# Optimization experiments

Measured on AMD Instinct MI355X. Metric: run time of the kernel, lower is better.

The kernel has to match this reference:

```python
import jax, jax.numpy as jnp
import numpy as np
from jax import lax

IMG_H = IMG_W = 800.0
PRE_NMS = 2000      # rpn_pre_nms_top_n (test)
POST_NMS = 1000     # rpn_post_nms_top_n (test)
IOU_THR = 0.7       # rpn nms_thresh
MIN_SIZE = 1e-3     # filter_proposals min_size
SCORE_THR = 0.0     # rpn score_thresh
BBOX_CLIP = float(np.log(1000.0 / 16.0))  # torchvision BoxCoder bbox_xform_clip


def setup_inputs() -> dict:
    key = jax.random.key(0)
    k1, k2, k3, k4 = jax.random.split(key, 4)
    N, A = 8, 1_000_000
    objectness = jax.random.normal(k1, (N, A), jnp.float32)
    deltas = jax.random.normal(k2, (N, A, 4), jnp.float32) * 0.5
    # realistic anchors: random centers inside the image, sizes in [16, 256]
    cxy = jax.random.uniform(k3, (A, 2), jnp.float32) * jnp.array([IMG_W, IMG_H], jnp.float32)
    wh = 16.0 + jax.random.uniform(k4, (A, 2), jnp.float32) * 240.0
    anchors = jnp.concatenate([cxy - 0.5 * wh, cxy + 0.5 * wh], axis=-1)
    return {"objectness": objectness, "deltas": deltas, "anchors": anchors}


def decode_boxes(deltas, anchors):
    # torchvision BoxCoder.decode_single with weights (1,1,1,1)
    wa = anchors[:, 2] - anchors[:, 0]          # [A]
    ha = anchors[:, 3] - anchors[:, 1]
    cxa = anchors[:, 0] + 0.5 * wa
    cya = anchors[:, 1] + 0.5 * ha
    dx, dy = deltas[..., 0], deltas[..., 1]      # [N, A]
    dw = jnp.minimum(deltas[..., 2], BBOX_CLIP)
    dh = jnp.minimum(deltas[..., 3], BBOX_CLIP)
    pcx = dx * wa + cxa
    pcy = dy * ha + cya
    pw = jnp.exp(dw) * wa
    ph = jnp.exp(dh) * ha
    return jnp.stack([pcx - 0.5 * pw, pcy - 0.5 * ph,
                      pcx + 0.5 * pw, pcy + 0.5 * ph], axis=-1)  # [N, A, 4]


def nms_keep(boxes, valid):
    # greedy NMS on score-sorted boxes [K,4]; returns boolean keep mask [K]
    K = boxes.shape[0]
    areas = (boxes[:, 2] - boxes[:, 0]) * (boxes[:, 3] - boxes[:, 1])
    idxs = jnp.arange(K)

    def body(i, keep):
        xx1 = jnp.maximum(boxes[i, 0], boxes[:, 0])
        yy1 = jnp.maximum(boxes[i, 1], boxes[:, 1])
        xx2 = jnp.minimum(boxes[i, 2], boxes[:, 2])
        yy2 = jnp.minimum(boxes[i, 3], boxes[:, 3])
        inter = jnp.maximum(xx2 - xx1, 0.0) * jnp.maximum(yy2 - yy1, 0.0)
        iou = inter / (areas[i] + areas - inter + 1e-12)
        sup = (iou > IOU_THR) & (idxs > i) & keep[i]
        return keep & ~sup

    return lax.fori_loop(0, K, body, valid)


def filter_one(obj, boxes):
    # per-image filter_proposals: top-k -> sigmoid -> clip -> small-box removal -> NMS -> top post_nms
    top_logits, idx = lax.top_k(obj, PRE_NMS)        # sorted desc; sigmoid is monotone
    b = boxes[idx]                                    # [K, 4]
    scores = jax.nn.sigmoid(top_logits)
    x1 = jnp.clip(b[:, 0], 0.0, IMG_W)
    y1 = jnp.clip(b[:, 1], 0.0, IMG_H)
    x2 = jnp.clip(b[:, 2], 0.0, IMG_W)
    y2 = jnp.clip(b[:, 3], 0.0, IMG_H)
    bc = jnp.stack([x1, y1, x2, y2], axis=-1)
    valid = ((x2 - x1) >= MIN_SIZE) & ((y2 - y1) >= MIN_SIZE) & (scores > SCORE_THR)
    keep = nms_keep(lax.stop_gradient(bc), valid)     # selection is non-differentiable
    masked = jnp.where(keep, scores, -jnp.inf)
    _, fidx = lax.top_k(lax.stop_gradient(masked), POST_NMS)
    out_boxes = bc[fidx]                              # [POST_NMS, 4]
    out_scores = jnp.where(keep[fidx], scores[fidx], 0.0)
    return out_boxes, out_scores


def reference(objectness, deltas, anchors):
    proposals = decode_boxes(deltas, anchors)                 # [N, A, 4]
    boxes, scores = jax.vmap(filter_one)(objectness, proposals)
    return jnp.concatenate([boxes, scores[:, :, None]], axis=-1)  # [N, POST_NMS, 5]
```

## Files before the change

kernel.cpp:

```cpp
#include <hip/hip_runtime.h>
#include <cstdint>

#define NIMG 8
#define PRE 2000
#define POST 1000
#define NCH 128
#define CH_CAP 128
#define CAND_TOT (NCH*CH_CAP)
#define NSORT 4
#define GPS (NCH/NSORT)
#define SEG 2048
#define CAND_MAX (NSORT*SEG)
#define NPB 64
#define PB_CAP 1024
#define PAIR_CAP 12288
#define JT 256
#define IMGW 800.0f
#define BBOX_CLIP_F 4.135166556742356f
#define STATIC_KMIN 0xC0200000u

#define OFF_BCNT  0
#define OFF_DONE  (OFF_BCNT + NIMG*NCH*4)
#define OFF_BPCNT (OFF_DONE + 1024)
#define OFF_CAND  (OFF_BPCNT + NIMG*NPB*4)
#define OFF_SRT   (OFF_CAND + (size_t)NIMG*CAND_TOT*8)
#define OFF_BOX   (OFF_SRT + (size_t)NIMG*CAND_MAX*8)
#define OFF_SCORE (OFF_BOX + (size_t)NIMG*PRE*16)
#define OFF_VALID (OFF_SCORE + NIMG*PRE*4)
#define OFF_PAIRS (OFF_VALID + NIMG*PRE*4)

__device__ __forceinline__ unsigned int fkey(float f) {
    unsigned int b = __float_as_uint(f);
    return (b & 0x80000000u) ? ~b : (b | 0x80000000u);
}
__device__ __forceinline__ float inv_fkey(unsigned int k) {
    unsigned int b = (k & 0x80000000u) ? (k ^ 0x80000000u) : ~k;
    return __uint_as_float(b);
}

__global__ void k_compact(const float* __restrict__ obj,
                          unsigned long long* __restrict__ cand,
                          unsigned int* __restrict__ bcnt,
                          unsigned int* __restrict__ done, int A) {
    __shared__ unsigned long long loc[CH_CAP];
    __shared__ unsigned int lcnt;
    const int img = blockIdx.y;
    const int b = blockIdx.x;
    const int t = threadIdx.x;
    if (t == 0) {
        lcnt = 0u;
        if (b == 0) done[img * 32] = 0u;
    }
    __syncthreads();
    const float4* p4 = (const float4*)(obj + (size_t)img * A);
    const int nvec = A >> 2;
    for (int i = b * 256 + t; i < nvec; i += NCH * 256) {
        float4 v = p4[i];
        unsigned int k0 = fkey(v.x), k1 = fkey(v.y), k2 = fkey(v.z), k3 = fkey(v.w);
        unsigned int base = (unsigned int)(i << 2);
        if (k0 >= STATIC_KMIN) { unsigned int p = atomicAdd(&lcnt, 1u); if (p < CH_CAP) loc[p] = ((unsigned long long)k0 << 32) | (0xFFFFFFFFu - base); }
        if (k1 >= STATIC_KMIN) { unsigned int p = atomicAdd(&lcnt, 1u); if (p < CH_CAP) loc[p] = ((unsigned long long)k1 << 32) | (0xFFFFFFFFu - (base + 1u)); }
        if (k2 >= STATIC_KMIN) { unsigned int p = atomicAdd(&lcnt, 1u); if (p < CH_CAP) loc[p] = ((unsigned long long)k2 << 32) | (0xFFFFFFFFu - (base + 2u)); }
        if (k3 >= STATIC_KMIN) { unsigned int p = atomicAdd(&lcnt, 1u); if (p < CH_CAP) loc[p] = ((unsigned long long)k3 << 32) | (0xFFFFFFFFu - (base + 3u)); }
    }
    if (b == 0) {
        const float* p = obj + (size_t)img * A;
        for (int i = (nvec << 2) + t; i < A; i += 256) {
            unsigned int k = fkey(p[i]);
            if (k >= STATIC_KMIN) { unsigned int q = atomicAdd(&lcnt, 1u); if (q < CH_CAP) loc[q] = ((unsigned long long)k << 32) | (0xFFFFFFFFu - (unsigned int)i); }
        }
    }
    __syncthreads();
    if (t == 0) bcnt[img * NCH + b] = lcnt;
    unsigned int n = min(lcnt, (unsigned int)CH_CAP);
    unsigned long long* dst = cand + (size_t)img * CAND_TOT + (size_t)b * CH_CAP;
    for (unsigned int i = t; i < n; i += 256) dst[i] = loc[i];
}

__global__ __launch_bounds__(1024) void k_sortmerge(
    const float* __restrict__ obj, const float* __restrict__ deltas, const float* __restrict__ anchors,
    unsigned long long* __restrict__ cand, const unsigned int* __restrict__ bcnt,
    unsigned long long* __restrict__ srt, unsigned int* __restrict__ done,
    float* __restrict__ boxes, float* __restrict__ scores, unsigned int* __restrict__ valid, int A) {
    __shared__ unsigned long long sb[3 * SEG];
    __shared__ unsigned int cnts[NCH];
    __shared__ unsigned int pref[GPS + 1];
    __shared__ unsigned int kth_s, lcnt;
    __shared__ int bad_s;
    const int img = blockIdx.y;
    const int myseg = blockIdx.x;
    const int t = threadIdx.x;

    if (t < NCH) cnts[t] = bcnt[img * NCH + t];
    __syncthreads();
    if (t == 0) {
        int bad = 0; unsigned int tot = 0;
        for (int c = 0; c < NCH; ++c) { unsigned int r = cnts[c]; if (r > CH_CAP) bad = 1; tot += min(r, (unsigned int)CH_CAP); }
        for (int g = 0; g < NSORT; ++g) {
            unsigned int s = 0;
            for (int c = 0; c < GPS; ++c) s += min(cnts[g * GPS + c], (unsigned int)CH_CAP);
            if (s > (unsigned int)SEG) bad = 1;
        }
        if (tot < (unsigned int)PRE) bad = 1;
        bad_s = bad;
        if (!bad) {
            unsigned int o = 0; pref[0] = 0;
            for (int c = 0; c < GPS; ++c) { o += min(cnts[myseg * GPS + c], (unsigned int)CH_CAP); pref[c + 1] = o; }
        }
    }
    __syncthreads();

    for (int i = t; i < SEG; i += 1024) sb[i] = 0ull;
    __syncthreads();

    if (!bad_s) {
        const int c = t >> 5, lane = t & 31;
        const unsigned int b0 = pref[c], n = pref[c + 1] - pref[c];
        const unsigned long long* src = cand + (size_t)img * CAND_TOT + (size_t)(myseg * GPS + c) * CH_CAP;
        for (unsigned int i = lane; i < n; i += 32) sb[b0 + i] = src[i];
    } else {
        unsigned int* h = (unsigned int*)sb;
        for (int i = t; i < 4096; i += 1024) h[i] = 0u;
        __syncthreads();
        const float* p = obj + (size_t)img * A;
        for (int i = t; i < A; i += 1024) atomicAdd(&h[fkey(p[i]) >> 20], 1u);
        __syncthreads();
        if (t == 0) {
            unsigned int run = 0, kb = 0;
            for (int b = 4095; b >= 0; --b) { run += h[b]; if (run >= (unsigned int)PRE) { kb = (unsigned int)b; break; } }
            kth_s = kb << 20;
        }
        __syncthreads();
        for (int i = t; i < SEG; i += 1024) sb[i] = 0ull;
        if (t == 0) lcnt = 0u;
        __syncthreads();
        for (int i = t; i < A; i += 1024) {
            unsigned int k = fkey(p[i]);
            if (k >= kth_s && (i & (NSORT - 1)) == myseg) {
                unsigned int q = atomicAdd(&lcnt, 1u);
                if (q < (unsigned int)SEG)
                    sb[q] = ((unsigned long long)k << 32) | (0xFFFFFFFFu - (unsigned int)i);
            }
        }
    }
    __syncthreads();

    for (int k = 2; k <= SEG; k <<= 1) {
        for (int j = k >> 1; j > 0; j >>= 1) {
            for (int i = t; i < SEG; i += 1024) {
                int l = i ^ j;
                if (l > i) {
                    unsigned long long a = sb[i], b = sb[l];
                    bool sw = ((i & k) == 0) ? (a < b) : (a > b);
                    if (sw) { sb[i] = b; sb[l] = a; }
                }
            }
            __syncthreads();
        }
    }

    unsigned long long* seg_out = srt + (size_t)img * CAND_MAX + (size_t)myseg * SEG;
    for (int i = t; i < SEG; i += 1024) seg_out[i] = sb[i];
    __syncthreads();
    unsigned int* dn = done + img * 32;
    if (t == 0) {
        __threadfence();
        atomicAdd(dn, 1u);
        while (atomicAdd(dn, 0u) < (unsigned int)NSORT) __builtin_amdgcn_s_sleep(8);
    }
    __syncthreads();
    __threadfence();

    const unsigned long long* simg = srt + (size_t)img * CAND_MAX;
    {
        int q = 0;
        for (int s2 = 0; s2 < NSORT; ++s2) {
            if (s2 == myseg) continue;
            const unsigned long long* src = simg + (size_t)s2 * SEG;
            for (int i = t; i < SEG; i += 1024) sb[q * SEG + i] = src[i];
            ++q;
        }
    }
    __syncthreads();

    const unsigned long long* own = simg + (size_t)myseg * SEG;
    for (int e2 = t; e2 < SEG; e2 += 1024) {
        unsigned long long v = own[e2];
        if (v == 0ull) continue;
        int rank = e2;
#pragma unroll
        for (int q = 0; q < NSORT - 1; ++q) {
            int lo = 0, hi = SEG;
            const unsigned long long* seg = sb + q * SEG;
            while (lo < hi) {
                int mid = (lo + hi) >> 1;
                if (seg[mid] > v) lo = mid + 1; else hi = mid;
            }
            rank += lo;
        }
        if (rank >= PRE) continue;
        unsigned int idx = 0xFFFFFFFFu - (unsigned int)(v & 0xFFFFFFFFull);
        float logit = inv_fkey((unsigned int)(v >> 32));
        float4 d = ((const float4*)deltas)[(size_t)img * A + idx];
        float4 a = ((const float4*)anchors)[idx];
        float wa = a.z - a.x, ha = a.w - a.y;
        float cxa = a.x + 0.5f * wa, cya = a.y + 0.5f * ha;
        float dw = fminf(d.z, BBOX_CLIP_F), dh = fminf(d.w, BBOX_CLIP_F);
        float pcx = d.x * wa + cxa, pcy = d.y * ha + cya;
        float pw = expf(dw) * wa, ph = expf(dh) * ha;
        float x1 = fminf(fmaxf(pcx - 0.5f * pw, 0.0f), IMGW);
        float y1 = fminf(fmaxf(pcy - 0.5f * ph, 0.0f), IMGW);
        float x2 = fminf(fmaxf(pcx + 0.5f * pw, 0.0f), IMGW);
        float y2 = fminf(fmaxf(pcy + 0.5f * ph, 0.0f), IMGW);
        float sc = 1.0f / (1.0f + expf(-logit));
        unsigned int vd = (((x2 - x1) >= 1e-3f) && ((y2 - y1) >= 1e-3f) && (sc > 0.0f)) ? 1u : 0u;
        ((float4*)boxes)[(size_t)img * PRE + rank] = make_float4(x1, y1, x2, y2);
        scores[img * PRE + rank] = sc;
        valid[img * PRE + rank] = vd;
    }
}

__global__ void k_pairs(const float* __restrict__ boxes, unsigned int* __restrict__ pairs,
                        unsigned int* __restrict__ bpcnt) {
#pragma clang fp contract(off)
    const int img = blockIdx.y;
    const int bid = blockIdx.x;
    const int it = bid >> 3;
    const int jc = bid & 7;
    const int t = threadIdx.x;
    if (jc < it) { if (t == 0) bpcnt[img * NPB + bid] = 0u; return; }
    __shared__ float4 jb[JT];
    __shared__ float jar[JT];
    __shared__ unsigned int lp[PB_CAP];
    __shared__ unsigned int lcnt;
    if (t == 0) lcnt = 0u;
    const float4* B = (const float4*)(boxes + (size_t)img * PRE * 4);
    const int j0 = jc * JT;
    const int jn = min(JT, PRE - j0);
    if (t < jn) {
        float4 b = B[j0 + t];
        jb[t] = b;
        jar[t] = (b.z - b.x) * (b.w - b.y);
    }
    const int i = it * JT + t;
    const bool row_ok = (i < PRE);
    float x1 = 0, y1 = 0, x2 = 0, y2 = 0, ai = 0;
    if (row_ok) {
        float4 b = B[i];
        x1 = b.x; y1 = b.y; x2 = b.z; y2 = b.w;
        ai = (b.z - b.x) * (b.w - b.y);
    }
    __syncthreads();
    if (row_ok) {
#pragma unroll 4
        for (int jj = 0; jj < jn; ++jj) {
            float4 bj = jb[jj];
            float aj = jar[jj];
            float xx1 = fmaxf(x1, bj.x);
            float yy1 = fmaxf(y1, bj.y);
            float xx2 = fminf(x2, bj.z);
            float yy2 = fminf(y2, bj.w);
            float iw = fmaxf(xx2 - xx1, 0.0f);
            float ih = fmaxf(yy2 - yy1, 0.0f);
            float inter = iw * ih;
            float iou = inter / (ai + aj - inter + 1e-12f);
            int j = j0 + jj;
            if (iou > 0.7f && j > i) {
                unsigned int p = atomicAdd(&lcnt, 1u);
                if (p < PB_CAP) lp[p] = ((unsigned int)i << 11) | (unsigned int)j;
            }
        }
    }
    __syncthreads();
    unsigned int n = min(lcnt, (unsigned int)PB_CAP);
    if (t == 0) bpcnt[img * NPB + bid] = n;
    unsigned int* dst = pairs + ((size_t)img * NPB + bid) * PB_CAP;
    for (unsigned int q = t; q < n; q += blockDim.x) dst[q] = lp[q];
}

__global__ __launch_bounds__(1024) void k_final(
    const float* __restrict__ boxes, const float* __restrict__ scores, const unsigned int* __restrict__ valid,
    const unsigned int* __restrict__ pairs, const unsigned int* __restrict__ bpcnt, float* __restrict__ out) {
    __shared__ unsigned int pb[PAIR_CAP];
    __shared__ unsigned int bp[NPB];
    __shared__ unsigned int ofs[NPB + 1];
    __shared__ unsigned char vld[2048];
    __shared__ unsigned char alive[2048];
    __shared__ unsigned char kill[2048];
    __shared__ unsigned int incl[2048];
    __shared__ int changed;
    const int img = blockIdx.x;
    const int t = threadIdx.x;
    if (t < NPB) bp[t] = min(bpcnt[img * NPB + t], (unsigned int)PB_CAP);
    __syncthreads();
    if (t == 0) {
        unsigned int o = 0; ofs[0] = 0;
        for (int c = 0; c < NPB; ++c) { o += bp[c]; if (o > (unsigned int)PAIR_CAP) o = PAIR_CAP; ofs[c + 1] = o; }
    }
    for (int i = t; i < 2048; i += 1024) {
        unsigned char v = (i < PRE) ? (unsigned char)valid[img * PRE + i] : 0;
        vld[i] = v;
        alive[i] = v;
    }
    __syncthreads();
    for (int c = 0; c < NPB; ++c) {
        unsigned int b0 = ofs[c], n = ofs[c + 1] - ofs[c];
        const unsigned int* src = pairs + ((size_t)img * NPB + c) * PB_CAP;
        for (unsigned int i = t; i < n; i += 1024) pb[b0 + i] = src[i];
    }
    const int np = (int)ofs[NPB];
    __syncthreads();
    for (int iter = 0; iter < 2048; ++iter) {
        if (t == 0) changed = 0;
        for (int i = t; i < 2048; i += 1024) kill[i] = 0;
        __syncthreads();
        for (int e = t; e < np; e += 1024) {
            unsigned int u = pb[e];
            unsigned int i = u >> 11, j = u & 2047u;
            if (alive[i]) kill[j] = 1;
        }
        __syncthreads();
        for (int i = t; i < 2048; i += 1024) {
            unsigned char na = (vld[i] && !kill[i]) ? 1 : 0;
            if (na != alive[i]) { alive[i] = na; changed = 1; }
        }
        __syncthreads();
        bool done = (changed == 0);
        __syncthreads();
        if (done) break;
    }
    const int i0 = t, i1 = t + 1024;
    incl[i0] = alive[i0]; incl[i1] = alive[i1];
    __syncthreads();
    for (int d = 1; d < 2048; d <<= 1) {
        unsigned int v0 = (i0 >= d) ? incl[i0 - d] : 0u;
        unsigned int v1 = (i1 >= d) ? incl[i1 - d] : 0u;
        __syncthreads();
        incl[i0] += v0; incl[i1] += v1;
        __syncthreads();
    }
    const unsigned int Nk = incl[2047];
    for (int i = t; i < PRE; i += 1024) {
        int slot = -1;
        float sc = 0.0f;
        if (alive[i]) {
            unsigned int r = incl[i] - 1u;
            if (r < (unsigned int)POST) { slot = (int)r; sc = scores[img * PRE + i]; }
        } else if (Nk < (unsigned int)POST) {
            unsigned int rnk = (unsigned int)i - incl[i];
            unsigned int s2 = Nk + rnk;
            if (s2 < (unsigned int)POST) { slot = (int)s2; sc = 0.0f; }
        }
        if (slot >= 0) {
            float4 b = ((const float4*)boxes)[(size_t)img * PRE + i];
            float* o = out + ((size_t)img * POST + slot) * 5;
            o[0] = b.x; o[1] = b.y; o[2] = b.z; o[3] = b.w; o[4] = sc;
        }
    }
}

extern "C" void kernel_launch(void* const* d_in, const int* in_sizes, int n_in,
                              void* d_out, int out_size, void* d_ws, size_t ws_size,
                              hipStream_t stream) {
    const float* obj = (const float*)d_in[0];
    const float* deltas = (const float*)d_in[1];
    const float* anchors = (const float*)d_in[2];
    float* out = (float*)d_out;
    const int A = in_sizes[0] / NIMG;

    char* ws = (char*)d_ws;
    unsigned int* bcnt = (unsigned int*)(ws + OFF_BCNT);
    unsigned int* done = (unsigned int*)(ws + OFF_DONE);
    unsigned int* bpcnt = (unsigned int*)(ws + OFF_BPCNT);
    unsigned long long* cand = (unsigned long long*)(ws + OFF_CAND);
    unsigned long long* srt = (unsigned long long*)(ws + OFF_SRT);
    float* boxes = (float*)(ws + OFF_BOX);
    float* scores = (float*)(ws + OFF_SCORE);
    unsigned int* valid = (unsigned int*)(ws + OFF_VALID);
    unsigned int* pairs = (unsigned int*)(ws + OFF_PAIRS);

    k_compact<<<dim3(NCH, NIMG), dim3(256), 0, stream>>>(obj, cand, bcnt, done, A);
    k_sortmerge<<<dim3(NSORT, NIMG), dim3(1024), 0, stream>>>(obj, deltas, anchors, cand, bcnt, srt, done, boxes, scores, valid, A);
    k_pairs<<<dim3(NPB, NIMG), dim3(256), 0, stream>>>(boxes, pairs, bpcnt);
    k_final<<<dim3(NIMG), dim3(1024), 0, stream>>>(boxes, scores, valid, pairs, bpcnt, out);
}
```

Baseline: 304.7 us.

## Split sort/merge into separate kernels and launch only upper-triangle pair tiles

Replaces the in-kernel spin-wait barrier between the four sort blocks with a kernel boundary, so sorting and the merge/decode step run as separate launches and the global done counter goes away. The pairs kernel now launches only the 36 upper-triangle tile blocks instead of 64 blocks that mostly returned early. The compaction uses 64 chunks of capacity 256 instead of 128 of 128, halving compaction blocks per image. The cost is one extra kernel launch and a re-read of the sorted segments from global memory.

```diff
diff --git a/kernel.cpp b/kernel.cpp
--- a/kernel.cpp
+++ b/kernel.cpp
@@ -4,14 +4,14 @@
 #define NIMG 8
 #define PRE 2000
 #define POST 1000
-#define NCH 128
-#define CH_CAP 128
+#define NCH 64
+#define CH_CAP 256
 #define CAND_TOT (NCH*CH_CAP)
 #define NSORT 4
 #define GPS (NCH/NSORT)
 #define SEG 2048
 #define CAND_MAX (NSORT*SEG)
-#define NPB 64
+#define NPT 36
 #define PB_CAP 1024
 #define PAIR_CAP 12288
 #define JT 256
@@ -20,9 +20,8 @@
 #define STATIC_KMIN 0xC0200000u
 
 #define OFF_BCNT  0
-#define OFF_DONE  (OFF_BCNT + NIMG*NCH*4)
-#define OFF_BPCNT (OFF_DONE + 1024)
-#define OFF_CAND  (OFF_BPCNT + NIMG*NPB*4)
+#define OFF_BPCNT (OFF_BCNT + NIMG*NCH*4)
+#define OFF_CAND  (OFF_BPCNT + NIMG*64*4)
 #define OFF_SRT   (OFF_CAND + (size_t)NIMG*CAND_TOT*8)
 #define OFF_BOX   (OFF_SRT + (size_t)NIMG*CAND_MAX*8)
 #define OFF_SCORE (OFF_BOX + (size_t)NIMG*PRE*16)
@@ -40,17 +39,13 @@
 
 __global__ void k_compact(const float* __restrict__ obj,
                           unsigned long long* __restrict__ cand,
-                          unsigned int* __restrict__ bcnt,
-                          unsigned int* __restrict__ done, int A) {
+                          unsigned int* __restrict__ bcnt, int A) {
     __shared__ unsigned long long loc[CH_CAP];
     __shared__ unsigned int lcnt;
     const int img = blockIdx.y;
     const int b = blockIdx.x;
     const int t = threadIdx.x;
-    if (t == 0) {
-        lcnt = 0u;
-        if (b == 0) done[img * 32] = 0u;
-    }
+    if (t == 0) lcnt = 0u;
     __syncthreads();
     const float4* p4 = (const float4*)(obj + (size_t)img * A);
     const int nvec = A >> 2;
@@ -77,12 +72,10 @@
     for (unsigned int i = t; i < n; i += 256) dst[i] = loc[i];
 }
 
-__global__ __launch_bounds__(1024) void k_sortmerge(
-    const float* __restrict__ obj, const float* __restrict__ deltas, const float* __restrict__ anchors,
-    unsigned long long* __restrict__ cand, const unsigned int* __restrict__ bcnt,
-    unsigned long long* __restrict__ srt, unsigned int* __restrict__ done,
-    float* __restrict__ boxes, float* __restrict__ scores, unsigned int* __restrict__ valid, int A) {
-    __shared__ unsigned long long sb[3 * SEG];
+__global__ __launch_bounds__(1024) void k_sort(
+    const float* __restrict__ obj, const unsigned long long* __restrict__ cand,
+    const unsigned int* __restrict__ bcnt, unsigned long long* __restrict__ srt, int A) {
+    __shared__ unsigned long long sb[SEG];
     __shared__ unsigned int cnts[NCH];
     __shared__ unsigned int pref[GPS + 1];
     __shared__ unsigned int kth_s, lcnt;
@@ -109,15 +102,14 @@
         }
     }
     __syncthreads();
-
     for (int i = t; i < SEG; i += 1024) sb[i] = 0ull;
     __syncthreads();
 
     if (!bad_s) {
-        const int c = t >> 5, lane = t & 31;
+        const int c = t >> 6, lane = t & 63;
         const unsigned int b0 = pref[c], n = pref[c + 1] - pref[c];
         const unsigned long long* src = cand + (size_t)img * CAND_TOT + (size_t)(myseg * GPS + c) * CH_CAP;
-        for (unsigned int i = lane; i < n; i += 32) sb[b0 + i] = src[i];
+        for (unsigned int i = lane; i < n; i += 64) sb[b0 + i] = src[i];
     } else {
         unsigned int* h = (unsigned int*)sb;
         for (int i = t; i < 4096; i += 1024) h[i] = 0u;
@@ -158,40 +150,31 @@
             __syncthreads();
         }
     }
-
-    unsigned long long* seg_out = srt + (size_t)img * CAND_MAX + (size_t)myseg * SEG;
-    for (int i = t; i < SEG; i += 1024) seg_out[i] = sb[i];
-    __syncthreads();
-    unsigned int* dn = done + img * 32;
-    if (t == 0) {
-        __threadfence();
-        atomicAdd(dn, 1u);
-        while (atomicAdd(dn, 0u) < (unsigned int)NSORT) __builtin_amdgcn_s_sleep(8);
-    }
-    __syncthreads();
-    __threadfence();
-
-    const unsigned long long* simg = srt + (size_t)img * CAND_MAX;
-    {
-        int q = 0;
-        for (int s2 = 0; s2 < NSORT; ++s2) {
-            if (s2 == myseg) continue;
-            const unsigned long long* src = simg + (size_t)s2 * SEG;
-            for (int i = t; i < SEG; i += 1024) sb[q * SEG + i] = src[i];
-            ++q;
-        }
-    }
-    __syncthreads();
-
-    const unsigned long long* own = simg + (size_t)myseg * SEG;
+    unsigned long long* dst = srt + (size_t)img * CAND_MAX + (size_t)myseg * SEG;
+    for (int i = t; i < SEG; i += 1024) dst[i] = sb[i];
+}
+
+__global__ __launch_bounds__(1024) void k_merge_decode(
+    const float* __restrict__ deltas, const float* __restrict__ anchors,
+    const unsigned long long* __restrict__ srt,
+    float* __restrict__ boxes, float* __restrict__ scores, unsigned int* __restrict__ valid, int A) {
+    __shared__ unsigned long long sb[CAND_MAX];
+    const int img = blockIdx.y;
+    const int myseg = blockIdx.x;
+    const int t = threadIdx.x;
+    const unsigned long long* c = srt + (size_t)img * CAND_MAX;
+    for (int i = t; i < CAND_MAX; i += 1024) sb[i] = c[i];
+    __syncthreads();
     for (int e2 = t; e2 < SEG; e2 += 1024) {
-        unsigned long long v = own[e2];
+        const int e = (myseg << 11) + e2;
+        unsigned long long v = sb[e];
         if (v == 0ull) continue;
         int rank = e2;
 #pragma unroll
-        for (int q = 0; q < NSORT - 1; ++q) {
+        for (int s = 0; s < 4; ++s) {
+            if (s == myseg) continue;
             int lo = 0, hi = SEG;
-            const unsigned long long* seg = sb + q * SEG;
+            const unsigned long long* seg = sb + (s << 11);
             while (lo < hi) {
                 int mid = (lo + hi) >> 1;
                 if (seg[mid] > v) lo = mid + 1; else hi = mid;
@@ -225,10 +208,10 @@
 #pragma clang fp contract(off)
     const int img = blockIdx.y;
     const int bid = blockIdx.x;
-    const int it = bid >> 3;
-    const int jc = bid & 7;
-    const int t = threadIdx.x;
-    if (jc < it) { if (t == 0) bpcnt[img * NPB + bid] = 0u; return; }
+    int rem = bid, it = 0;
+    while (rem >= 8 - it) { rem -= 8 - it; ++it; }
+    const int jc = it + rem;
+    const int t = threadIdx.x;
     __shared__ float4 jb[JT];
     __shared__ float jar[JT];
     __shared__ unsigned int lp[PB_CAP];
@@ -273,8 +256,8 @@
     }
     __syncthreads();
     unsigned int n = min(lcnt, (unsigned int)PB_CAP);
-    if (t == 0) bpcnt[img * NPB + bid] = n;
-    unsigned int* dst = pairs + ((size_t)img * NPB + bid) * PB_CAP;
+    if (t == 0) bpcnt[img * 64 + bid] = n;
+    unsigned int* dst = pairs + ((size_t)img * NPT + bid) * PB_CAP;
     for (unsigned int q = t; q < n; q += blockDim.x) dst[q] = lp[q];
 }
 
@@ -282,8 +265,8 @@
     const float* __restrict__ boxes, const float* __restrict__ scores, const unsigned int* __restrict__ valid,
     const unsigned int* __restrict__ pairs, const unsigned int* __restrict__ bpcnt, float* __restrict__ out) {
     __shared__ unsigned int pb[PAIR_CAP];
-    __shared__ unsigned int bp[NPB];
-    __shared__ unsigned int ofs[NPB + 1];
+    __shared__ unsigned int bp[NPT];
+    __shared__ unsigned int ofs[NPT + 1];
     __shared__ unsigned char vld[2048];
     __shared__ unsigned char alive[2048];
     __shared__ unsigned char kill[2048];
@@ -291,11 +274,11 @@
     __shared__ int changed;
     const int img = blockIdx.x;
     const int t = threadIdx.x;
-    if (t < NPB) bp[t] = min(bpcnt[img * NPB + t], (unsigned int)PB_CAP);
+    if (t < NPT) bp[t] = min(bpcnt[img * 64 + t], (unsigned int)PB_CAP);
     __syncthreads();
     if (t == 0) {
         unsigned int o = 0; ofs[0] = 0;
-        for (int c = 0; c < NPB; ++c) { o += bp[c]; if (o > (unsigned int)PAIR_CAP) o = PAIR_CAP; ofs[c + 1] = o; }
+        for (int c = 0; c < NPT; ++c) { o += bp[c]; if (o > (unsigned int)PAIR_CAP) o = PAIR_CAP; ofs[c + 1] = o; }
     }
     for (int i = t; i < 2048; i += 1024) {
         unsigned char v = (i < PRE) ? (unsigned char)valid[img * PRE + i] : 0;
@@ -303,12 +286,12 @@
         alive[i] = v;
     }
     __syncthreads();
-    for (int c = 0; c < NPB; ++c) {
+    for (int c = 0; c < NPT; ++c) {
         unsigned int b0 = ofs[c], n = ofs[c + 1] - ofs[c];
-        const unsigned int* src = pairs + ((size_t)img * NPB + c) * PB_CAP;
+        const unsigned int* src = pairs + ((size_t)img * NPT + c) * PB_CAP;
         for (unsigned int i = t; i < n; i += 1024) pb[b0 + i] = src[i];
     }
-    const int np = (int)ofs[NPB];
+    const int np = (int)ofs[NPT];
     __syncthreads();
     for (int iter = 0; iter < 2048; ++iter) {
         if (t == 0) changed = 0;
@@ -370,7 +353,6 @@
 
     char* ws = (char*)d_ws;
     unsigned int* bcnt = (unsigned int*)(ws + OFF_BCNT);
-    unsigned int* done = (unsigned int*)(ws + OFF_DONE);
     unsigned int* bpcnt = (unsigned int*)(ws + OFF_BPCNT);
     unsigned long long* cand = (unsigned long long*)(ws + OFF_CAND);
     unsigned long long* srt = (unsigned long long*)(ws + OFF_SRT);
@@ -379,8 +361,9 @@
     unsigned int* valid = (unsigned int*)(ws + OFF_VALID);
     unsigned int* pairs = (unsigned int*)(ws + OFF_PAIRS);
 
-    k_compact<<<dim3(NCH, NIMG), dim3(256), 0, stream>>>(obj, cand, bcnt, done, A);
-    k_sortmerge<<<dim3(NSORT, NIMG), dim3(1024), 0, stream>>>(obj, deltas, anchors, cand, bcnt, srt, done, boxes, scores, valid, A);
-    k_pairs<<<dim3(NPB, NIMG), dim3(256), 0, stream>>>(boxes, pairs, bpcnt);
+    k_compact<<<dim3(NCH, NIMG), dim3(256), 0, stream>>>(obj, cand, bcnt, A);
+    k_sort<<<dim3(NSORT, NIMG), dim3(1024), 0, stream>>>(obj, cand, bcnt, srt, A);
+    k_merge_decode<<<dim3(NSORT, NIMG), dim3(1024), 0, stream>>>(deltas, anchors, srt, boxes, scores, valid, A);
+    k_pairs<<<dim3(NPT, NIMG), dim3(256), 0, stream>>>(boxes, pairs, bpcnt);
     k_final<<<dim3(NIMG), dim3(1024), 0, stream>>>(boxes, scores, valid, pairs, bpcnt, out);
 }
```

New measurement: 292.7 us. 1.04x faster.
